# Optimization experiments

Measured on AMD Instinct MI355X. Metric: run time of the kernel, lower is better.

The kernel has to match this reference:

```python
import jax, jax.numpy as jnp
import numpy as np
import math

HIDDEN = 2048
N_HEADS = 32
N_KV_HEADS = 8
HEAD_DIM = HIDDEN // N_HEADS  # 64
N_REP = N_HEADS // N_KV_HEADS  # 4
ROPE_THETA = 10000.0
BSZ, SEQ = 2, 2048


def setup_inputs() -> dict:
    key = jax.random.key(0)
    ks = jax.random.split(key, 6)
    hidden_states = jax.random.normal(ks[0], (BSZ, SEQ, HIDDEN), dtype=jnp.float32)
    wq = jax.random.normal(ks[1], (HIDDEN, N_HEADS * HEAD_DIM), dtype=jnp.float32) * (HIDDEN ** -0.5)
    wk = jax.random.normal(ks[2], (HIDDEN, N_KV_HEADS * HEAD_DIM), dtype=jnp.float32) * (HIDDEN ** -0.5)
    wv = jax.random.normal(ks[3], (HIDDEN, N_KV_HEADS * HEAD_DIM), dtype=jnp.float32) * (HIDDEN ** -0.5)
    wo = jax.random.normal(ks[4], (N_HEADS * HEAD_DIM, HIDDEN), dtype=jnp.float32) * (HIDDEN ** -0.5)
    # additive causal mask [b, 1, q, kv]
    neg = jnp.finfo(jnp.float32).min
    causal = jnp.where(jnp.tril(jnp.ones((SEQ, SEQ), dtype=bool)), 0.0, neg)
    attention_mask = jnp.broadcast_to(causal[None, None], (BSZ, 1, SEQ, SEQ)).astype(jnp.float32)
    position_ids = jnp.broadcast_to(jnp.arange(SEQ, dtype=jnp.int32)[None], (BSZ, SEQ))
    return {
        "hidden_states": hidden_states,
        "wq": wq, "wk": wk, "wv": wv, "wo": wo,
        "attention_mask": attention_mask,
        "position_ids": position_ids,
    }


def _rope_cache(seq_len, dtype):
    inv_freq = 1.0 / (ROPE_THETA ** (jnp.arange(0, HEAD_DIM, 2, dtype=jnp.float32) / HEAD_DIM))
    t = jnp.arange(seq_len, dtype=jnp.float32)
    freqs = jnp.outer(t, inv_freq)              # [S, head_dim/2]
    emb = jnp.concatenate([freqs, freqs], -1)   # [S, head_dim]
    return jnp.cos(emb).astype(dtype), jnp.sin(emb).astype(dtype)


def _rotate_half(x):
    x1, x2 = jnp.split(x, 2, axis=-1)
    return jnp.concatenate([-x2, x1], axis=-1)


def reference(hidden_states, wq, wk, wv, wo, attention_mask, position_ids):
    b, s, _ = hidden_states.shape
    q = (hidden_states @ wq).reshape(b, s, N_HEADS, HEAD_DIM).transpose(0, 2, 1, 3)
    k = (hidden_states @ wk).reshape(b, s, N_KV_HEADS, HEAD_DIM).transpose(0, 2, 1, 3)
    v = (hidden_states @ wv).reshape(b, s, N_KV_HEADS, HEAD_DIM).transpose(0, 2, 1, 3)

    cos_c, sin_c = _rope_cache(s, hidden_states.dtype)
    cos = cos_c[position_ids][:, None]  # [b,1,s,head_dim]
    sin = sin_c[position_ids][:, None]
    q = q * cos + _rotate_half(q) * sin
    k = k * cos + _rotate_half(k) * sin

    # repeat_kv: [b, kvh, s, d] -> [b, kvh*n_rep, s, d]
    k = jnp.broadcast_to(k[:, :, None], (b, N_KV_HEADS, N_REP, s, HEAD_DIM)).reshape(b, N_HEADS, s, HEAD_DIM)
    v = jnp.broadcast_to(v[:, :, None], (b, N_KV_HEADS, N_REP, s, HEAD_DIM)).reshape(b, N_HEADS, s, HEAD_DIM)

    scores = jnp.einsum('bhqd,bhkd->bhqk', q, k) / math.sqrt(HEAD_DIM)
    scores = scores + attention_mask
    probs = jax.nn.softmax(scores.astype(jnp.float32), axis=-1).astype(q.dtype)
    attn = jnp.einsum('bhqk,bhkd->bhqd', probs, v)  # [b,h,s,d]
    attn = attn.transpose(0, 2, 1, 3).reshape(b, s, N_HEADS * HEAD_DIM)
    return attn @ wo
```

## Files before the change

### kernel.cpp

```cpp
#include <hip/hip_runtime.h>
#include <math.h>


typedef float f32x4 __attribute__((ext_vector_type(4)));
typedef short s16x8 __attribute__((ext_vector_type(8)));
typedef unsigned short u16x4 __attribute__((ext_vector_type(4)));

__device__ __forceinline__ unsigned short f2bf(float x) {
    union { float f; unsigned int u; } v; v.f = x;
    unsigned int r = v.u + 0x7FFF + ((v.u >> 16) & 1);
    return (unsigned short)(r >> 16);
}

__global__ __launch_bounds__(256) void prep(
    const float* __restrict__ X, const float* __restrict__ Wq,
    const float* __restrict__ Wk, const float* __restrict__ Wv,
    const float* __restrict__ Wo,
    unsigned short* __restrict__ Xb, unsigned short* __restrict__ Wqkvt,
    unsigned short* __restrict__ Wot) {
    const int bid = blockIdx.x;
    if (bid < 8192) {
        size_t i = (size_t)bid * 256 + threadIdx.x;
        f32x4 v = *(const f32x4*)&X[i * 4];
        u16x4 r;
        r[0] = f2bf(v[0]); r[1] = f2bf(v[1]); r[2] = f2bf(v[2]); r[3] = f2bf(v[3]);
        *(u16x4*)&Xb[i * 4] = r;
        return;
    }
    __shared__ float t[32][33];
    const int tb = bid - 8192;
    const int kbi = tb / 160, bx = tb - kbi * 160;
    const float* W; unsigned short* Out; int N, n0, nb;
    if (bx < 64)      { W = Wq; Out = Wqkvt; N = 2048; n0 = 0;    nb = bx; }
    else if (bx < 80) { W = Wk; Out = Wqkvt; N = 512;  n0 = 2048; nb = bx - 64; }
    else if (bx < 96) { W = Wv; Out = Wqkvt; N = 512;  n0 = 2560; nb = bx - 80; }
    else              { W = Wo; Out = Wot;   N = 2048; n0 = 0;    nb = bx - 96; }
    int kb = kbi * 32; nb *= 32;
    int tx = threadIdx.x & 31, ty = threadIdx.x >> 5;
#pragma unroll
    for (int i = 0; i < 4; ++i)
        t[ty + i * 8][tx] = W[(size_t)(kb + ty + i * 8) * N + nb + tx];
    __syncthreads();
#pragma unroll
    for (int i = 0; i < 4; ++i)
        Out[(size_t)(n0 + nb + ty + i * 8) * 2048 + kb + tx] = f2bf(t[tx][ty + i * 8]);
}

__global__ __launch_bounds__(384, 3) void gemm_qkv_rope(
    const unsigned short* __restrict__ A, const unsigned short* __restrict__ Bt,
    const int* __restrict__ pos,
    unsigned short* __restrict__ Qb, unsigned short* __restrict__ Kb,
    unsigned short* __restrict__ Vt) {
    const int K = 2048;
    const int NKT = 32;
    __shared__ unsigned short As[2][128 * 64];
    __shared__ unsigned short Bs[2][192 * 64];
    const int tid = threadIdx.x;
    const int wave = tid >> 6, lane = tid & 63;
    const int col = lane & 15, quad = lane >> 4;

    const int lin = blockIdx.y * 16 + blockIdx.x;
    const int xcd = lin & 7, t8 = lin >> 3;
    const int bx = (xcd & 1) * 8 + (t8 & 7);
    const int by = (xcd >> 1) * 8 + (t8 >> 3);
    const int m0 = by * 128, n0 = bx * 192;
    const int wrow = wave / 3, wcol = wave - wrow * 3;
    const int wm = wrow * 64, wn = wcol * 64;

    const int lrow = lane >> 3;
    const int gch = (lane & 7) ^ lrow;
    const unsigned short* Ag = A + (size_t)(m0 + lrow) * K + gch * 8;
    const unsigned short* Bg = Bt + (size_t)(n0 + lrow) * K + gch * 8;

    const int aid0 = wave, aid1 = wave + 6;
    const int aid2 = (wave + 12 < 16) ? wave + 12 : wave - 4;

#define STAGE_T(buf, kt)                                                       \
    {                                                                          \
        __builtin_amdgcn_global_load_lds(                                      \
            (const __attribute__((address_space(1))) void*)(Ag + (size_t)aid0 * 8 * K + (size_t)(kt) * 64), \
            (__attribute__((address_space(3))) void*)(&As[buf][aid0 * 512]), 16, 0, 0); \
        __builtin_amdgcn_global_load_lds(                                      \
            (const __attribute__((address_space(1))) void*)(Ag + (size_t)aid1 * 8 * K + (size_t)(kt) * 64), \
            (__attribute__((address_space(3))) void*)(&As[buf][aid1 * 512]), 16, 0, 0); \
        __builtin_amdgcn_global_load_lds(                                      \
            (const __attribute__((address_space(1))) void*)(Ag + (size_t)aid2 * 8 * K + (size_t)(kt) * 64), \
            (__attribute__((address_space(3))) void*)(&As[buf][aid2 * 512]), 16, 0, 0); \
        _Pragma("unroll")                                                      \
        for (int j = 0; j < 4; ++j) {                                          \
            const int bid = wave + j * 6;                                      \
            __builtin_amdgcn_global_load_lds(                                  \
                (const __attribute__((address_space(1))) void*)(Bg + (size_t)bid * 8 * K + (size_t)(kt) * 64), \
                (__attribute__((address_space(3))) void*)(&Bs[buf][bid * 512]), 16, 0, 0); \
        }                                                                      \
    }
#define RD_A(buf, mi, ks)                                                      \
    (*(const s16x8*)&As[buf][(wm + (mi) * 16 + col) * 64 +                     \
                             ((((ks) << 2) + quad) ^ (col & 7)) * 8])
#define RD_B(buf, ni, ks)                                                      \
    (*(const s16x8*)&Bs[buf][(wn + (ni) * 16 + col) * 64 +                     \
                             ((((ks) << 2) + quad) ^ (col & 7)) * 8])

    s16x8 a[2][2], b[4][2];
    f32x4 acc[4][4] = {};

    STAGE_T(0, 0);
    STAGE_T(1, 1);
    asm volatile("s_waitcnt vmcnt(7)" ::: "memory");
    __builtin_amdgcn_s_barrier();

    for (int t = 0; t < NKT; ++t) {
        const int p = t & 1;
#pragma unroll
        for (int mi = 0; mi < 2; ++mi) { a[mi][0] = RD_A(p, mi, 0); a[mi][1] = RD_A(p, mi, 1); }
#pragma unroll
        for (int ni = 0; ni < 4; ++ni) { b[ni][0] = RD_B(p, ni, 0); b[ni][1] = RD_B(p, ni, 1); }
        __builtin_amdgcn_s_barrier();
        asm volatile("s_waitcnt lgkmcnt(0)" ::: "memory");
        __builtin_amdgcn_s_setprio(1);
#pragma unroll
        for (int mi = 0; mi < 2; ++mi)
#pragma unroll
            for (int ni = 0; ni < 4; ++ni) {
                acc[mi][ni] = __builtin_amdgcn_mfma_f32_16x16x32_bf16(a[mi][0], b[ni][0], acc[mi][ni], 0, 0, 0);
                acc[mi][ni] = __builtin_amdgcn_mfma_f32_16x16x32_bf16(a[mi][1], b[ni][1], acc[mi][ni], 0, 0, 0);
            }
        __builtin_amdgcn_s_setprio(0);
        __builtin_amdgcn_s_barrier();
#pragma unroll
        for (int mi = 0; mi < 2; ++mi) { a[mi][0] = RD_A(p, 2 + mi, 0); a[mi][1] = RD_A(p, 2 + mi, 1); }
        __builtin_amdgcn_s_barrier();
        asm volatile("s_waitcnt lgkmcnt(0)" ::: "memory");
        if (t + 2 < NKT) STAGE_T(p, t + 2);
        __builtin_amdgcn_s_setprio(1);
#pragma unroll
        for (int mi = 0; mi < 2; ++mi)
#pragma unroll
            for (int ni = 0; ni < 4; ++ni) {
                acc[2 + mi][ni] = __builtin_amdgcn_mfma_f32_16x16x32_bf16(a[mi][0], b[ni][0], acc[2 + mi][ni], 0, 0, 0);
                acc[2 + mi][ni] = __builtin_amdgcn_mfma_f32_16x16x32_bf16(a[mi][1], b[ni][1], acc[2 + mi][ni], 0, 0, 0);
            }
        __builtin_amdgcn_s_setprio(0);
        if (t + 2 < NKT) asm volatile("s_waitcnt vmcnt(7)" ::: "memory");
        else             asm volatile("s_waitcnt vmcnt(0)" ::: "memory");
        __builtin_amdgcn_s_barrier();
    }
#undef STAGE_T
#undef RD_A
#undef RD_B

    const int cb = n0 + wn;
    if (cb >= 2560) {
        const int hd = (cb - 2560) >> 6;
#pragma unroll
        for (int mi = 0; mi < 4; ++mi) {
            int mb = m0 + wm + mi * 16 + quad * 4;
            int b = mb >> 11, s0 = mb & 2047;
#pragma unroll
            for (int ni = 0; ni < 4; ++ni) {
                u16x4 v;
#pragma unroll
                for (int r = 0; r < 4; ++r) v[r] = f2bf(acc[mi][ni][r]);
                *(u16x4*)&Vt[((size_t)(b * 8 + hd) * 64 + ni * 16 + col) * 2048 + s0] = v;
            }
        }
    } else {
        const int isQ = (cb < 2048);
        const int hd = isQ ? (cb >> 6) : ((cb - 2048) >> 6);
        const int nh = isQ ? 32 : 8;
        const float scale = isQ ? 0.125f : 1.0f;
        unsigned short* Out = isQ ? Qb : Kb;
        const float NEG_LN_TH_32 = -0.28782313662425575f;
        const float inv0 = __expf((float)col * NEG_LN_TH_32);
        const float inv1 = __expf((float)(col + 16) * NEG_LN_TH_32);
#pragma unroll
        for (int mi = 0; mi < 4; ++mi)
#pragma unroll
            for (int r = 0; r < 4; ++r) {
                int m = m0 + wm + mi * 16 + quad * 4 + r;
                int b = m >> 11, s = m & 2047;
                float p = (float)pos[m];
                float sn0, cs0, sn1, cs1;
                __sincosf(p * inv0, &sn0, &cs0);
                __sincosf(p * inv1, &sn1, &cs1);
                float a0 = acc[mi][0][r], a1 = acc[mi][1][r];
                float b0 = acc[mi][2][r], b1 = acc[mi][3][r];
                size_t rb = ((size_t)(b * nh + hd) * 2048 + s) * 64;
                Out[rb + col]      = f2bf((a0 * cs0 - b0 * sn0) * scale);
                Out[rb + col + 16] = f2bf((a1 * cs1 - b1 * sn1) * scale);
                Out[rb + col + 32] = f2bf((b0 * cs0 + a0 * sn0) * scale);
                Out[rb + col + 48] = f2bf((b1 * cs1 + a1 * sn1) * scale);
            }
    }
}

__global__ __launch_bounds__(256) void gemm_bf16_nt(
    const unsigned short* __restrict__ A, const unsigned short* __restrict__ Bt,
    float* __restrict__ C, int K, int ldc) {
    __shared__ unsigned short As[128 * 64];
    __shared__ unsigned short Bs[128 * 64];
    const int tid = threadIdx.x;
    const int wave = tid >> 6, lane = tid & 63;
    const int col = lane & 15, quad = lane >> 4;
    const int lin = blockIdx.y * 16 + blockIdx.x;
    const int xcd = lin & 7, t6 = lin >> 3;
    const int bx = (xcd & 1) * 8 + (t6 & 7);
    const int by = (xcd >> 1) * 8 + (t6 >> 3);
    const int m0 = by * 128, n0 = bx * 128;
    const int wm = (wave >> 1) * 64, wn = (wave & 1) * 64;

    const int lrow = lane >> 3;
    const int gch = (lane & 7) ^ lrow;
    const unsigned short* Ag = A + (size_t)(m0 + wave * 32 + lrow) * K + gch * 8;
    const unsigned short* Bg = Bt + (size_t)(n0 + wave * 32 + lrow) * K + gch * 8;
    unsigned short* AsW = As + wave * 2048;
    unsigned short* BsW = Bs + wave * 2048;

    f32x4 acc[4][4] = {};

    for (int k0 = 0; k0 < K; k0 += 64) {
#pragma unroll
        for (int i = 0; i < 4; ++i) {
            __builtin_amdgcn_global_load_lds(
                (const __attribute__((address_space(1))) void*)(Ag + (size_t)i * 8 * K + k0),
                (__attribute__((address_space(3))) void*)(AsW + i * 512), 16, 0, 0);
            __builtin_amdgcn_global_load_lds(
                (const __attribute__((address_space(1))) void*)(Bg + (size_t)i * 8 * K + k0),
                (__attribute__((address_space(3))) void*)(BsW + i * 512), 16, 0, 0);
        }
        __syncthreads();
#pragma unroll
        for (int ks = 0; ks < 2; ++ks) {
            const int slot = ((ks << 2) + quad) ^ (col & 7);
            s16x8 af[4], bf[4];
#pragma unroll
            for (int mi = 0; mi < 4; ++mi)
                af[mi] = *(const s16x8*)&As[(wm + mi * 16 + col) * 64 + slot * 8];
#pragma unroll
            for (int ni = 0; ni < 4; ++ni)
                bf[ni] = *(const s16x8*)&Bs[(wn + ni * 16 + col) * 64 + slot * 8];
#pragma unroll
            for (int mi = 0; mi < 4; ++mi)
#pragma unroll
                for (int ni = 0; ni < 4; ++ni)
                    acc[mi][ni] = __builtin_amdgcn_mfma_f32_16x16x32_bf16(
                        af[mi], bf[ni], acc[mi][ni], 0, 0, 0);
        }
        __syncthreads();
    }
#pragma unroll
    for (int mi = 0; mi < 4; ++mi)
#pragma unroll
        for (int ni = 0; ni < 4; ++ni)
#pragma unroll
            for (int r = 0; r < 4; ++r) {
                int m = m0 + wm + mi * 16 + quad * 4 + r;
                int n = n0 + wn + ni * 16 + col;
                C[(size_t)m * ldc + n] = acc[mi][ni][r];
            }
}

__global__ __launch_bounds__(128, 2) void flash_attn(
    const unsigned short* __restrict__ Qb, const unsigned short* __restrict__ Kb,
    const unsigned short* __restrict__ Vt, unsigned short* __restrict__ Ob) {
    __shared__ unsigned short Ks[64 * 64];
    __shared__ unsigned short Vs[64 * 64];
    __shared__ unsigned short PsA[2][32 * 64];
    __shared__ unsigned short PsB[2][32 * 64];

    const int tid = threadIdx.x;
    const int wave = tid >> 6, lane = tid & 63;
    const int col = lane & 15, quad = lane >> 4;

    const int id = blockIdx.x;
    const int j = ((id & 15) + ((id >> 8) << 2)) & 15;
    const int bh = id >> 4;
    const int b = bh >> 5, h = bh & 31, kvh = h >> 2;
    const int qA0 = (31 - j) * 64, qB0 = j * 64;
    const int qwA = qA0 + wave * 32, qwB = qB0 + wave * 32;

    const unsigned short* Qg  = Qb + ((size_t)(b * 32 + h) * 2048) * 64;
    const unsigned short* Kgb = Kb + ((size_t)(b * 8 + kvh) * 2048) * 64;
    const unsigned short* Vgb = Vt + ((size_t)(b * 8 + kvh) * 64) * 2048;

    const int r8 = lane >> 3, g = (lane & 7) ^ r8;
    const unsigned short* KgL = Kgb + (size_t)(wave * 32 + r8) * 64 + g * 8;
    const unsigned short* VgL = Vgb + (size_t)(wave * 32 + r8) * 2048 + g * 8;
    unsigned short* KsW = Ks + wave * 32 * 64;
    unsigned short* VsW = Vs + wave * 32 * 64;

    const s16x8 onesf = {16256, 16256, 16256, 16256, 16256, 16256, 16256, 16256};

    s16x8 qfA[2][2], qfB[2][2];
#pragma unroll
    for (int qc = 0; qc < 2; ++qc)
#pragma unroll
        for (int ks = 0; ks < 2; ++ks) {
            qfA[qc][ks] = *(const s16x8*)&Qg[(size_t)(qwA + qc * 16 + col) * 64 + ks * 32 + quad * 8];
            qfB[qc][ks] = *(const s16x8*)&Qg[(size_t)(qwB + qc * 16 + col) * 64 + ks * 32 + quad * 8];
        }

    f32x4 aoA[2][4] = {}, aoB[2][4] = {};
    f32x4 alA[2] = {}, alB[2] = {};

    for (int kv0 = 0; kv0 <= qA0; kv0 += 64) {
#pragma unroll
        for (int i = 0; i < 4; ++i) {
            __builtin_amdgcn_global_load_lds(
                (const __attribute__((address_space(1))) void*)(KgL + (size_t)(kv0 + i * 8) * 64),
                (__attribute__((address_space(3))) void*)(KsW + i * 512), 16, 0, 0);
            __builtin_amdgcn_global_load_lds(
                (const __attribute__((address_space(1))) void*)(VgL + kv0 + (size_t)i * 8 * 2048),
                (__attribute__((address_space(3))) void*)(VsW + i * 512), 16, 0, 0);
        }
        __syncthreads();
        const bool doB = (kv0 <= qB0);
#pragma unroll
        for (int mi = 0; mi < 4; ++mi) {
            const int s0 = quad ^ (col & 7);
            const int s1 = (4 + quad) ^ (col & 7);
            s16x8 kf0 = *(const s16x8*)&Ks[(mi * 16 + col) * 64 + s0 * 8];
            s16x8 kf1 = *(const s16x8*)&Ks[(mi * 16 + col) * 64 + s1 * 8];
            const int chl = (mi * 2 + (quad >> 1)) ^ (col & 7);
#pragma unroll
            for (int qc = 0; qc < 2; ++qc) {
                f32x4 sc = {};
                sc = __builtin_amdgcn_mfma_f32_16x16x32_bf16(kf0, qfA[qc][0], sc, 0, 0, 0);
                sc = __builtin_amdgcn_mfma_f32_16x16x32_bf16(kf1, qfA[qc][1], sc, 0, 0, 0);
                if (kv0 == qA0) {
                    int kvb = kv0 + mi * 16 + quad * 4, q = qwA + qc * 16 + col;
#pragma unroll
                    for (int r = 0; r < 4; ++r)
                        if (kvb + r > q) sc[r] = -1e30f;
                }
                unsigned eb[4];
#pragma unroll
                for (int r = 0; r < 4; ++r) eb[r] = __float_as_uint(__expf(sc[r]));
                uint2 pk;
                pk.x = __builtin_amdgcn_perm(eb[1], eb[0], 0x07060302u);
                pk.y = __builtin_amdgcn_perm(eb[3], eb[2], 0x07060302u);
                *(uint2*)&PsA[wave][(qc * 16 + col) * 64 + chl * 8 + (quad & 1) * 4] = pk;
            }
            if (doB) {
#pragma unroll
                for (int qc = 0; qc < 2; ++qc) {
                    f32x4 sc = {};
                    sc = __builtin_amdgcn_mfma_f32_16x16x32_bf16(kf0, qfB[qc][0], sc, 0, 0, 0);
                    sc = __builtin_amdgcn_mfma_f32_16x16x32_bf16(kf1, qfB[qc][1], sc, 0, 0, 0);
                    if (kv0 == qB0) {
                        int kvb = kv0 + mi * 16 + quad * 4, q = qwB + qc * 16 + col;
#pragma unroll
                        for (int r = 0; r < 4; ++r)
                            if (kvb + r > q) sc[r] = -1e30f;
                    }
                    unsigned eb[4];
#pragma unroll
                    for (int r = 0; r < 4; ++r) eb[r] = __float_as_uint(__expf(sc[r]));
                    uint2 pk;
                    pk.x = __builtin_amdgcn_perm(eb[1], eb[0], 0x07060302u);
                    pk.y = __builtin_amdgcn_perm(eb[3], eb[2], 0x07060302u);
                    *(uint2*)&PsB[wave][(qc * 16 + col) * 64 + chl * 8 + (quad & 1) * 4] = pk;
                }
            }
        }
        asm volatile("s_waitcnt lgkmcnt(0)" ::: "memory");
#pragma unroll
        for (int ks = 0; ks < 2; ++ks) {
            const int slot = ((ks << 2) + quad) ^ (col & 7);
            s16x8 vf[4];
#pragma unroll
            for (int di = 0; di < 4; ++di)
                vf[di] = *(const s16x8*)&Vs[(di * 16 + col) * 64 + slot * 8];
#pragma unroll
            for (int qc = 0; qc < 2; ++qc) {
                s16x8 pfA = *(const s16x8*)&PsA[wave][(qc * 16 + col) * 64 + slot * 8];
                alA[qc] = __builtin_amdgcn_mfma_f32_16x16x32_bf16(pfA, onesf, alA[qc], 0, 0, 0);
#pragma unroll
                for (int di = 0; di < 4; ++di)
                    aoA[qc][di] = __builtin_amdgcn_mfma_f32_16x16x32_bf16(pfA, vf[di], aoA[qc][di], 0, 0, 0);
            }
            if (doB) {
#pragma unroll
                for (int qc = 0; qc < 2; ++qc) {
                    s16x8 pfB = *(const s16x8*)&PsB[wave][(qc * 16 + col) * 64 + slot * 8];
                    alB[qc] = __builtin_amdgcn_mfma_f32_16x16x32_bf16(pfB, onesf, alB[qc], 0, 0, 0);
#pragma unroll
                    for (int di = 0; di < 4; ++di)
                        aoB[qc][di] = __builtin_amdgcn_mfma_f32_16x16x32_bf16(pfB, vf[di], aoB[qc][di], 0, 0, 0);
                }
            }
        }
        __syncthreads();
    }

#pragma unroll
    for (int qc = 0; qc < 2; ++qc)
#pragma unroll
        for (int r = 0; r < 4; ++r) {
            {
                int qg = qwA + qc * 16 + quad * 4 + r;
                float inv = 1.f / alA[qc][r];
                size_t base = ((size_t)b * 2048 + qg) * 2048 + h * 64;
#pragma unroll
                for (int di = 0; di < 4; ++di)
                    Ob[base + di * 16 + col] = f2bf(aoA[qc][di][r] * inv);
            }
            {
                int qg = qwB + qc * 16 + quad * 4 + r;
                float inv = 1.f / alB[qc][r];
                size_t base = ((size_t)b * 2048 + qg) * 2048 + h * 64;
#pragma unroll
                for (int di = 0; di < 4; ++di)
                    Ob[base + di * 16 + col] = f2bf(aoB[qc][di][r] * inv);
            }
        }
}

extern "C" void kernel_launch(void* const* d_in, const int* in_sizes, int n_in,
                              void* d_out, int out_size, void* d_ws, size_t ws_size,
                              hipStream_t stream) {
    const float* X  = (const float*)d_in[0];
    const float* Wq = (const float*)d_in[1];
    const float* Wk = (const float*)d_in[2];
    const float* Wv = (const float*)d_in[3];
    const float* Wo = (const float*)d_in[4];
    const int* pos  = (const int*)d_in[6];
    float* out = (float*)d_out;

    char* ws = (char*)d_ws;
    unsigned short* Xb    = (unsigned short*)(ws + 0);
    unsigned short* Wqkvt = (unsigned short*)(ws + 16777216);
    unsigned short* Wot   = (unsigned short*)(ws + 29360128);
    unsigned short* Qb    = (unsigned short*)(ws + 37748736);
    unsigned short* Kb    = (unsigned short*)(ws + 54525952);
    unsigned short* Vt    = (unsigned short*)(ws + 62914560);
    unsigned short* Attn  = Xb;

    prep<<<18432, 256, 0, stream>>>(X, Wq, Wk, Wv, Wo, Xb, Wqkvt, Wot);
    gemm_qkv_rope<<<dim3(16, 32), 384, 0, stream>>>(Xb, Wqkvt, pos, Qb, Kb, Vt);
    flash_attn<<<1024, 128, 0, stream>>>(Qb, Kb, Vt, Attn);
    gemm_bf16_nt<<<dim3(16, 32), 256, 0, stream>>>(Attn, Wot, out, 2048, 2048);
}
```

Before: 318.0 us.

## Stage QKV GEMM tiles through registers and unroll double-buffer loop

```diff
diff --git a/kernel.cpp b/kernel.cpp
--- a/kernel.cpp
+++ b/kernel.cpp
@@ -74,26 +74,26 @@
 
     const int aid0 = wave, aid1 = wave + 6;
     const int aid2 = (wave + 12 < 16) ? wave + 12 : wave - 4;
-
-#define STAGE_T(buf, kt)                                                       \
-    {                                                                          \
-        __builtin_amdgcn_global_load_lds(                                      \
-            (const __attribute__((address_space(1))) void*)(Ag + (size_t)aid0 * 8 * K + (size_t)(kt) * 64), \
-            (__attribute__((address_space(3))) void*)(&As[buf][aid0 * 512]), 16, 0, 0); \
-        __builtin_amdgcn_global_load_lds(                                      \
-            (const __attribute__((address_space(1))) void*)(Ag + (size_t)aid1 * 8 * K + (size_t)(kt) * 64), \
-            (__attribute__((address_space(3))) void*)(&As[buf][aid1 * 512]), 16, 0, 0); \
-        __builtin_amdgcn_global_load_lds(                                      \
-            (const __attribute__((address_space(1))) void*)(Ag + (size_t)aid2 * 8 * K + (size_t)(kt) * 64), \
-            (__attribute__((address_space(3))) void*)(&As[buf][aid2 * 512]), 16, 0, 0); \
-        _Pragma("unroll")                                                      \
-        for (int j = 0; j < 4; ++j) {                                          \
-            const int bid = wave + j * 6;                                      \
-            __builtin_amdgcn_global_load_lds(                                  \
-                (const __attribute__((address_space(1))) void*)(Bg + (size_t)bid * 8 * K + (size_t)(kt) * 64), \
-                (__attribute__((address_space(3))) void*)(&Bs[buf][bid * 512]), 16, 0, 0); \
-        }                                                                      \
-    }
+    const int bid0 = wave, bid1 = wave + 6, bid2 = wave + 12, bid3 = wave + 18;
+
+#define ISSUE_T(A0, A1, A2, B0, B1, B2, B3, kt)                                \
+    A0 = *(const uint4*)(Ag + (size_t)aid0 * 8 * K + (size_t)(kt) * 64);       \
+    A1 = *(const uint4*)(Ag + (size_t)aid1 * 8 * K + (size_t)(kt) * 64);       \
+    A2 = *(const uint4*)(Ag + (size_t)aid2 * 8 * K + (size_t)(kt) * 64);       \
+    B0 = *(const uint4*)(Bg + (size_t)bid0 * 8 * K + (size_t)(kt) * 64);       \
+    B1 = *(const uint4*)(Bg + (size_t)bid1 * 8 * K + (size_t)(kt) * 64);       \
+    B2 = *(const uint4*)(Bg + (size_t)bid2 * 8 * K + (size_t)(kt) * 64);       \
+    B3 = *(const uint4*)(Bg + (size_t)bid3 * 8 * K + (size_t)(kt) * 64);
+
+#define WRITE_T(buf, A0, A1, A2, B0, B1, B2, B3)                               \
+    *(uint4*)&As[buf][aid0 * 512 + lane * 8] = A0;                             \
+    *(uint4*)&As[buf][aid1 * 512 + lane * 8] = A1;                             \
+    *(uint4*)&As[buf][aid2 * 512 + lane * 8] = A2;                             \
+    *(uint4*)&Bs[buf][bid0 * 512 + lane * 8] = B0;                             \
+    *(uint4*)&Bs[buf][bid1 * 512 + lane * 8] = B1;                             \
+    *(uint4*)&Bs[buf][bid2 * 512 + lane * 8] = B2;                             \
+    *(uint4*)&Bs[buf][bid3 * 512 + lane * 8] = B3;
+
 #define RD_A(buf, mi, ks)                                                      \
     (*(const s16x8*)&As[buf][(wm + (mi) * 16 + col) * 64 +                     \
                              ((((ks) << 2) + quad) ^ (col & 7)) * 8])
@@ -103,49 +103,64 @@
 
     s16x8 a[2][2], b[4][2];
     f32x4 acc[4][4] = {};
-
-    STAGE_T(0, 0);
-    STAGE_T(1, 1);
+    uint4 s0a0, s0a1, s0a2, s0b0, s0b1, s0b2, s0b3;
+    uint4 s1a0, s1a1, s1a2, s1b0, s1b1, s1b2, s1b3;
+
+    ISSUE_T(s0a0, s0a1, s0a2, s0b0, s0b1, s0b2, s0b3, 0);
+    ISSUE_T(s1a0, s1a1, s1a2, s1b0, s1b1, s1b2, s1b3, 1);
     asm volatile("s_waitcnt vmcnt(7)" ::: "memory");
+    WRITE_T(0, s0a0, s0a1, s0a2, s0b0, s0b1, s0b2, s0b3);
+    asm volatile("s_waitcnt vmcnt(0)" ::: "memory");
+    WRITE_T(1, s1a0, s1a1, s1a2, s1b0, s1b1, s1b2, s1b3);
+    asm volatile("s_waitcnt lgkmcnt(0)" ::: "memory");
     __builtin_amdgcn_s_barrier();
 
-    for (int t = 0; t < NKT; ++t) {
-        const int p = t & 1;
-#pragma unroll
-        for (int mi = 0; mi < 2; ++mi) { a[mi][0] = RD_A(p, mi, 0); a[mi][1] = RD_A(p, mi, 1); }
-#pragma unroll
-        for (int ni = 0; ni < 4; ++ni) { b[ni][0] = RD_B(p, ni, 0); b[ni][1] = RD_B(p, ni, 1); }
-        __builtin_amdgcn_s_barrier();
-        asm volatile("s_waitcnt lgkmcnt(0)" ::: "memory");
-        __builtin_amdgcn_s_setprio(1);
-#pragma unroll
-        for (int mi = 0; mi < 2; ++mi)
-#pragma unroll
-            for (int ni = 0; ni < 4; ++ni) {
-                acc[mi][ni] = __builtin_amdgcn_mfma_f32_16x16x32_bf16(a[mi][0], b[ni][0], acc[mi][ni], 0, 0, 0);
-                acc[mi][ni] = __builtin_amdgcn_mfma_f32_16x16x32_bf16(a[mi][1], b[ni][1], acc[mi][ni], 0, 0, 0);
-            }
-        __builtin_amdgcn_s_setprio(0);
-        __builtin_amdgcn_s_barrier();
-#pragma unroll
-        for (int mi = 0; mi < 2; ++mi) { a[mi][0] = RD_A(p, 2 + mi, 0); a[mi][1] = RD_A(p, 2 + mi, 1); }
-        __builtin_amdgcn_s_barrier();
-        asm volatile("s_waitcnt lgkmcnt(0)" ::: "memory");
-        if (t + 2 < NKT) STAGE_T(p, t + 2);
-        __builtin_amdgcn_s_setprio(1);
-#pragma unroll
-        for (int mi = 0; mi < 2; ++mi)
-#pragma unroll
-            for (int ni = 0; ni < 4; ++ni) {
-                acc[2 + mi][ni] = __builtin_amdgcn_mfma_f32_16x16x32_bf16(a[mi][0], b[ni][0], acc[2 + mi][ni], 0, 0, 0);
-                acc[2 + mi][ni] = __builtin_amdgcn_mfma_f32_16x16x32_bf16(a[mi][1], b[ni][1], acc[2 + mi][ni], 0, 0, 0);
-            }
-        __builtin_amdgcn_s_setprio(0);
-        if (t + 2 < NKT) asm volatile("s_waitcnt vmcnt(7)" ::: "memory");
-        else             asm volatile("s_waitcnt vmcnt(0)" ::: "memory");
-        __builtin_amdgcn_s_barrier();
-    }
-#undef STAGE_T
+#define TILE_BODY(P, PN, SA0, SA1, SA2, SB0, SB1, SB2, SB3,                    \
+                  WA0, WA1, WA2, WB0, WB1, WB2, WB3, t)                        \
+    {                                                                          \
+        _Pragma("unroll")                                                      \
+        for (int mi = 0; mi < 2; ++mi) { a[mi][0] = RD_A(P, mi, 0); a[mi][1] = RD_A(P, mi, 1); } \
+        _Pragma("unroll")                                                      \
+        for (int ni = 0; ni < 4; ++ni) { b[ni][0] = RD_B(P, ni, 0); b[ni][1] = RD_B(P, ni, 1); } \
+        asm volatile("s_waitcnt lgkmcnt(0)" ::: "memory");                     \
+        __builtin_amdgcn_s_setprio(1);                                         \
+        _Pragma("unroll")                                                      \
+        for (int mi = 0; mi < 2; ++mi)                                         \
+            _Pragma("unroll")                                                  \
+            for (int ni = 0; ni < 4; ++ni) {                                   \
+                acc[mi][ni] = __builtin_amdgcn_mfma_f32_16x16x32_bf16(a[mi][0], b[ni][0], acc[mi][ni], 0, 0, 0); \
+                acc[mi][ni] = __builtin_amdgcn_mfma_f32_16x16x32_bf16(a[mi][1], b[ni][1], acc[mi][ni], 0, 0, 0); \
+            }                                                                  \
+        __builtin_amdgcn_s_setprio(0);                                         \
+        _Pragma("unroll")                                                      \
+        for (int mi = 0; mi < 2; ++mi) { a[mi][0] = RD_A(P, 2 + mi, 0); a[mi][1] = RD_A(P, 2 + mi, 1); } \
+        if ((t) + 2 < NKT) { ISSUE_T(SA0, SA1, SA2, SB0, SB1, SB2, SB3, (t) + 2) } \
+        asm volatile("s_waitcnt lgkmcnt(0)" ::: "memory");                     \
+        __builtin_amdgcn_s_setprio(1);                                         \
+        _Pragma("unroll")                                                      \
+        for (int mi = 0; mi < 2; ++mi)                                         \
+            _Pragma("unroll")                                                  \
+            for (int ni = 0; ni < 4; ++ni) {                                   \
+                acc[2 + mi][ni] = __builtin_amdgcn_mfma_f32_16x16x32_bf16(a[mi][0], b[ni][0], acc[2 + mi][ni], 0, 0, 0); \
+                acc[2 + mi][ni] = __builtin_amdgcn_mfma_f32_16x16x32_bf16(a[mi][1], b[ni][1], acc[2 + mi][ni], 0, 0, 0); \
+            }                                                                  \
+        __builtin_amdgcn_s_setprio(0);                                         \
+        if ((t) + 2 < NKT) { asm volatile("s_waitcnt vmcnt(7)" ::: "memory"); } \
+        else               { asm volatile("s_waitcnt vmcnt(0)" ::: "memory"); } \
+        if ((t) >= 1 && (t) + 1 < NKT) { WRITE_T(PN, WA0, WA1, WA2, WB0, WB1, WB2, WB3) } \
+        asm volatile("s_waitcnt lgkmcnt(0)" ::: "memory");                     \
+        __builtin_amdgcn_s_barrier();                                          \
+    }
+
+    for (int tt = 0; tt < NKT; tt += 2) {
+        TILE_BODY(0, 1, s0a0, s0a1, s0a2, s0b0, s0b1, s0b2, s0b3,
+                  s1a0, s1a1, s1a2, s1b0, s1b1, s1b2, s1b3, tt);
+        TILE_BODY(1, 0, s1a0, s1a1, s1a2, s1b0, s1b1, s1b2, s1b3,
+                  s0a0, s0a1, s0a2, s0b0, s0b1, s0b2, s0b3, tt + 1);
+    }
+#undef TILE_BODY
+#undef ISSUE_T
+#undef WRITE_T
 #undef RD_A
 #undef RD_B
 
@@ -155,13 +170,13 @@
 #pragma unroll
         for (int mi = 0; mi < 4; ++mi) {
             int mb = m0 + wm + mi * 16 + quad * 4;
-            int b = mb >> 11, s0 = mb & 2047;
+            int b2 = mb >> 11, s0 = mb & 2047;
 #pragma unroll
             for (int ni = 0; ni < 4; ++ni) {
                 u16x4 v;
 #pragma unroll
                 for (int r = 0; r < 4; ++r) v[r] = f2bf(acc[mi][ni][r]);
-                *(u16x4*)&Vt[((size_t)(b * 8 + hd) * 64 + ni * 16 + col) * 2048 + s0] = v;
+                *(u16x4*)&Vt[((size_t)(b2 * 8 + hd) * 64 + ni * 16 + col) * 2048 + s0] = v;
             }
         }
     } else {
@@ -178,14 +193,14 @@
 #pragma unroll
             for (int r = 0; r < 4; ++r) {
                 int m = m0 + wm + mi * 16 + quad * 4 + r;
-                int b = m >> 11, s = m & 2047;
+                int b2 = m >> 11, s = m & 2047;
                 float p = (float)pos[m];
                 float sn0, cs0, sn1, cs1;
                 __sincosf(p * inv0, &sn0, &cs0);
                 __sincosf(p * inv1, &sn1, &cs1);
                 float a0 = acc[mi][0][r], a1 = acc[mi][1][r];
                 float b0 = acc[mi][2][r], b1 = acc[mi][3][r];
-                size_t rb = ((size_t)(b * nh + hd) * 2048 + s) * 64;
+                size_t rb = ((size_t)(b2 * nh + hd) * 2048 + s) * 64;
                 Out[rb + col]      = f2bf((a0 * cs0 - b0 * sn0) * scale);
                 Out[rb + col + 16] = f2bf((a1 * cs1 - b1 * sn1) * scale);
                 Out[rb + col + 32] = f2bf((b0 * cs0 + a0 * sn0) * scale);
```

Result: slower. 433.5 us (+36.3%).

## Replace direct global-to-LDS loads with register-staged prefetch in QKV GEMM

Applied to the files above, without the earlier changes.

```diff
diff --git a/kernel.cpp b/kernel.cpp
--- a/kernel.cpp
+++ b/kernel.cpp
@@ -74,26 +74,8 @@
 
     const int aid0 = wave, aid1 = wave + 6;
     const int aid2 = (wave + 12 < 16) ? wave + 12 : wave - 4;
-
-#define STAGE_T(buf, kt)                                                       \
-    {                                                                          \
-        __builtin_amdgcn_global_load_lds(                                      \
-            (const __attribute__((address_space(1))) void*)(Ag + (size_t)aid0 * 8 * K + (size_t)(kt) * 64), \
-            (__attribute__((address_space(3))) void*)(&As[buf][aid0 * 512]), 16, 0, 0); \
-        __builtin_amdgcn_global_load_lds(                                      \
-            (const __attribute__((address_space(1))) void*)(Ag + (size_t)aid1 * 8 * K + (size_t)(kt) * 64), \
-            (__attribute__((address_space(3))) void*)(&As[buf][aid1 * 512]), 16, 0, 0); \
-        __builtin_amdgcn_global_load_lds(                                      \
-            (const __attribute__((address_space(1))) void*)(Ag + (size_t)aid2 * 8 * K + (size_t)(kt) * 64), \
-            (__attribute__((address_space(3))) void*)(&As[buf][aid2 * 512]), 16, 0, 0); \
-        _Pragma("unroll")                                                      \
-        for (int j = 0; j < 4; ++j) {                                          \
-            const int bid = wave + j * 6;                                      \
-            __builtin_amdgcn_global_load_lds(                                  \
-                (const __attribute__((address_space(1))) void*)(Bg + (size_t)bid * 8 * K + (size_t)(kt) * 64), \
-                (__attribute__((address_space(3))) void*)(&Bs[buf][bid * 512]), 16, 0, 0); \
-        }                                                                      \
-    }
+    const int bid0 = wave, bid1 = wave + 6, bid2 = wave + 12, bid3 = wave + 18;
+
 #define RD_A(buf, mi, ks)                                                      \
     (*(const s16x8*)&As[buf][(wm + (mi) * 16 + col) * 64 +                     \
                              ((((ks) << 2) + quad) ^ (col & 7)) * 8])
@@ -104,18 +86,44 @@
     s16x8 a[2][2], b[4][2];
     f32x4 acc[4][4] = {};
 
-    STAGE_T(0, 0);
-    STAGE_T(1, 1);
-    asm volatile("s_waitcnt vmcnt(7)" ::: "memory");
-    __builtin_amdgcn_s_barrier();
+    {
+        uint4 la0 = *(const uint4*)(Ag + (size_t)aid0 * 8 * K);
+        uint4 la1 = *(const uint4*)(Ag + (size_t)aid1 * 8 * K);
+        uint4 la2 = *(const uint4*)(Ag + (size_t)aid2 * 8 * K);
+        uint4 lb0 = *(const uint4*)(Bg + (size_t)bid0 * 8 * K);
+        uint4 lb1 = *(const uint4*)(Bg + (size_t)bid1 * 8 * K);
+        uint4 lb2 = *(const uint4*)(Bg + (size_t)bid2 * 8 * K);
+        uint4 lb3 = *(const uint4*)(Bg + (size_t)bid3 * 8 * K);
+        asm volatile("s_waitcnt vmcnt(0)" ::: "memory");
+        *(uint4*)&As[0][aid0 * 512 + lane * 8] = la0;
+        *(uint4*)&As[0][aid1 * 512 + lane * 8] = la1;
+        *(uint4*)&As[0][aid2 * 512 + lane * 8] = la2;
+        *(uint4*)&Bs[0][bid0 * 512 + lane * 8] = lb0;
+        *(uint4*)&Bs[0][bid1 * 512 + lane * 8] = lb1;
+        *(uint4*)&Bs[0][bid2 * 512 + lane * 8] = lb2;
+        *(uint4*)&Bs[0][bid3 * 512 + lane * 8] = lb3;
+        asm volatile("s_waitcnt lgkmcnt(0)" ::: "memory");
+        __builtin_amdgcn_s_barrier();
+    }
 
     for (int t = 0; t < NKT; ++t) {
         const int p = t & 1;
+        const bool nx = (t + 1 < NKT);
+        uint4 la0, la1, la2, lb0, lb1, lb2, lb3;
+        if (nx) {
+            const size_t ko = (size_t)(t + 1) * 64;
+            la0 = *(const uint4*)(Ag + (size_t)aid0 * 8 * K + ko);
+            la1 = *(const uint4*)(Ag + (size_t)aid1 * 8 * K + ko);
+            la2 = *(const uint4*)(Ag + (size_t)aid2 * 8 * K + ko);
+            lb0 = *(const uint4*)(Bg + (size_t)bid0 * 8 * K + ko);
+            lb1 = *(const uint4*)(Bg + (size_t)bid1 * 8 * K + ko);
+            lb2 = *(const uint4*)(Bg + (size_t)bid2 * 8 * K + ko);
+            lb3 = *(const uint4*)(Bg + (size_t)bid3 * 8 * K + ko);
+        }
 #pragma unroll
         for (int mi = 0; mi < 2; ++mi) { a[mi][0] = RD_A(p, mi, 0); a[mi][1] = RD_A(p, mi, 1); }
 #pragma unroll
         for (int ni = 0; ni < 4; ++ni) { b[ni][0] = RD_B(p, ni, 0); b[ni][1] = RD_B(p, ni, 1); }
-        __builtin_amdgcn_s_barrier();
         asm volatile("s_waitcnt lgkmcnt(0)" ::: "memory");
         __builtin_amdgcn_s_setprio(1);
 #pragma unroll
@@ -126,12 +134,9 @@
                 acc[mi][ni] = __builtin_amdgcn_mfma_f32_16x16x32_bf16(a[mi][1], b[ni][1], acc[mi][ni], 0, 0, 0);
             }
         __builtin_amdgcn_s_setprio(0);
-        __builtin_amdgcn_s_barrier();
 #pragma unroll
         for (int mi = 0; mi < 2; ++mi) { a[mi][0] = RD_A(p, 2 + mi, 0); a[mi][1] = RD_A(p, 2 + mi, 1); }
-        __builtin_amdgcn_s_barrier();
         asm volatile("s_waitcnt lgkmcnt(0)" ::: "memory");
-        if (t + 2 < NKT) STAGE_T(p, t + 2);
         __builtin_amdgcn_s_setprio(1);
 #pragma unroll
         for (int mi = 0; mi < 2; ++mi)
@@ -141,11 +146,20 @@
                 acc[2 + mi][ni] = __builtin_amdgcn_mfma_f32_16x16x32_bf16(a[mi][1], b[ni][1], acc[2 + mi][ni], 0, 0, 0);
             }
         __builtin_amdgcn_s_setprio(0);
-        if (t + 2 < NKT) asm volatile("s_waitcnt vmcnt(7)" ::: "memory");
-        else             asm volatile("s_waitcnt vmcnt(0)" ::: "memory");
+        if (nx) {
+            asm volatile("s_waitcnt vmcnt(0)" ::: "memory");
+            const int q = p ^ 1;
+            *(uint4*)&As[q][aid0 * 512 + lane * 8] = la0;
+            *(uint4*)&As[q][aid1 * 512 + lane * 8] = la1;
+            *(uint4*)&As[q][aid2 * 512 + lane * 8] = la2;
+            *(uint4*)&Bs[q][bid0 * 512 + lane * 8] = lb0;
+            *(uint4*)&Bs[q][bid1 * 512 + lane * 8] = lb1;
+            *(uint4*)&Bs[q][bid2 * 512 + lane * 8] = lb2;
+            *(uint4*)&Bs[q][bid3 * 512 + lane * 8] = lb3;
+            asm volatile("s_waitcnt lgkmcnt(0)" ::: "memory");
+        }
         __builtin_amdgcn_s_barrier();
     }
-#undef STAGE_T
 #undef RD_A
 #undef RD_B
 
@@ -155,13 +169,13 @@
 #pragma unroll
         for (int mi = 0; mi < 4; ++mi) {
             int mb = m0 + wm + mi * 16 + quad * 4;
-            int b = mb >> 11, s0 = mb & 2047;
+            int b2 = mb >> 11, s0 = mb & 2047;
 #pragma unroll
             for (int ni = 0; ni < 4; ++ni) {
                 u16x4 v;
 #pragma unroll
                 for (int r = 0; r < 4; ++r) v[r] = f2bf(acc[mi][ni][r]);
-                *(u16x4*)&Vt[((size_t)(b * 8 + hd) * 64 + ni * 16 + col) * 2048 + s0] = v;
+                *(u16x4*)&Vt[((size_t)(b2 * 8 + hd) * 64 + ni * 16 + col) * 2048 + s0] = v;
             }
         }
     } else {
@@ -178,14 +192,14 @@
 #pragma unroll
             for (int r = 0; r < 4; ++r) {
                 int m = m0 + wm + mi * 16 + quad * 4 + r;
-                int b = m >> 11, s = m & 2047;
+                int b2 = m >> 11, s = m & 2047;
                 float p = (float)pos[m];
                 float sn0, cs0, sn1, cs1;
                 __sincosf(p * inv0, &sn0, &cs0);
                 __sincosf(p * inv1, &sn1, &cs1);
                 float a0 = acc[mi][0][r], a1 = acc[mi][1][r];
                 float b0 = acc[mi][2][r], b1 = acc[mi][3][r];
-                size_t rb = ((size_t)(b * nh + hd) * 2048 + s) * 64;
+                size_t rb = ((size_t)(b2 * nh + hd) * 2048 + s) * 64;
                 Out[rb + col]      = f2bf((a0 * cs0 - b0 * sn0) * scale);
                 Out[rb + col + 16] = f2bf((a1 * cs1 - b1 * sn1) * scale);
                 Out[rb + col + 32] = f2bf((b0 * cs0 + a0 * sn0) * scale);
```

Result: no change. 316.7 us (-0.4%).
